# Kernel optimization log

Hardware: AMD Instinct MI355X
Metric: run time of the kernel (lower is better)

Reference implementation:

```python
import jax, jax.numpy as jnp
import numpy as np

N = 50000      # nodes
E = 1200000    # edges
G = 256        # graphs in batch
H = 64         # hidden_dim
F_IN = 5       # input_dim
L = 3          # num deep GCN layers
EPS_BN = 1e-5
EPS_MSG = 1e-7

def setup_inputs() -> dict:
    key = jax.random.key(0)
    ks = jax.random.split(key, 12)
    r = lambda i, shp, s=0.1: jax.random.normal(ks[i], shp, jnp.float32) * s
    return {
        "x": jax.random.normal(ks[0], (N, F_IN), jnp.float32),
        "edge_index": jax.random.randint(ks[1], (2, E), 0, N),
        "batch_idx": jnp.sort(jax.random.randint(ks[2], (N,), 0, G)),
        "conv1_W": r(3, (F_IN, H)), "conv1_b": jnp.zeros((H,), jnp.float32),
        "bn1_g": jnp.ones((H,), jnp.float32), "bn1_b": jnp.zeros((H,), jnp.float32),
        "ln_g": jnp.ones((L, H), jnp.float32), "ln_b": jnp.zeros((L, H), jnp.float32),
        "prelu_a": jnp.full((L, H), 0.25, jnp.float32),
        "gen_t": jnp.ones((L,), jnp.float32),
        "mlp_W1": r(4, (L, H, 2 * H)), "mlp_b1": jnp.zeros((L, 2 * H), jnp.float32),
        "mlp_bn_g": jnp.ones((L, 2 * H), jnp.float32), "mlp_bn_b": jnp.zeros((L, 2 * H), jnp.float32),
        "mlp_W2": r(5, (L, 2 * H, H)), "mlp_b2": jnp.zeros((L, H), jnp.float32),
        "lin1_W": r(6, ((L + 1) * H * 2, 2 * H)), "lin1_b": jnp.zeros((2 * H,), jnp.float32),
        "lin2_W": r(7, (2 * H, H)), "lin2_b": jnp.zeros((H,), jnp.float32),
        "out_W": r(8, (H, 1)), "out_b": jnp.zeros((1,), jnp.float32),
    }

def _layernorm(x, g, b):
    mu = jnp.mean(x, axis=-1, keepdims=True)
    var = jnp.mean(jnp.square(x - mu), axis=-1, keepdims=True)
    return (x - mu) * jax.lax.rsqrt(var + EPS_BN) * g + b

def _prelu(x, a):
    return jnp.where(x >= 0, x, a * x)

def _bn_eval(x, g, b):
    # eval-mode BatchNorm with running_mean=0, running_var=1
    return x * (g / jnp.sqrt(1.0 + EPS_BN)) + b

def reference(x, edge_index, batch_idx, conv1_W, conv1_b, bn1_g, bn1_b,
              ln_g, ln_b, prelu_a, gen_t, mlp_W1, mlp_b1, mlp_bn_g, mlp_bn_b,
              mlp_W2, mlp_b2, lin1_W, lin1_b, lin2_W, lin2_b, out_W, out_b):
    n = x.shape[0]
    src, dst = edge_index[0], edge_index[1]

    # ---- GCNConv (with self loops, symmetric normalization) ----
    loops = jnp.arange(n)
    row = jnp.concatenate([src, loops])  # [E+N]
    col = jnp.concatenate([dst, loops])
    h = x @ conv1_W
    deg = jax.ops.segment_sum(jnp.ones_like(col, jnp.float32), col, num_segments=n)
    dinv = jnp.where(deg > 0, deg ** -0.5, 0.0)
    norm = dinv[row] * dinv[col]
    h = jax.ops.segment_sum(h[row] * norm[:, None], col, num_segments=n) + conv1_b
    h = _bn_eval(h, bn1_g, bn1_b)
    h = jax.nn.relu(h)

    xs = [h]
    # ---- DeepGCNLayer (res+) x L, GENConv with softmax aggregation ----
    for i in range(ln_g.shape[0]):
        u = _layernorm(h, ln_g[i], ln_b[i])
        u = _prelu(u, prelu_a[i])
        msg = jax.nn.relu(u[src]) + EPS_MSG            # [E, H]
        sc = msg * gen_t[i]
        m = jax.ops.segment_max(sc, dst, num_segments=n)
        e = jnp.exp(sc - m[dst])
        s = jax.ops.segment_sum(e, dst, num_segments=n)
        alpha = e / s[dst]                             # segment-wise softmax per channel
        agg = jax.ops.segment_sum(msg * alpha, dst, num_segments=n) + u  # root add
        z = agg @ mlp_W1[i] + mlp_b1[i]
        z = _bn_eval(z, mlp_bn_g[i], mlp_bn_b[i])
        z = jax.nn.relu(z)
        z = z @ mlp_W2[i] + mlp_b2[i]
        h = h + z                                      # res+
        xs.append(h)

    # ---- JumpingKnowledge cat + global mean/max pool ----
    xc = jnp.concatenate(xs, axis=1)                   # [N, 4H]
    cnt = jax.ops.segment_sum(jnp.ones((n,), jnp.float32), batch_idx, num_segments=G)
    xmean = jax.ops.segment_sum(xc, batch_idx, num_segments=G) / jnp.maximum(cnt, 1.0)[:, None]
    xmax = jax.ops.segment_max(xc, batch_idx, num_segments=G)
    xmax = jnp.where(jnp.isfinite(xmax), xmax, 0.0)
    p = jnp.concatenate([xmean, xmax], axis=1)         # [G, 8H]

    # ---- readout MLP (dropout off in eval) ----
    p = jax.nn.relu(p @ lin1_W + lin1_b)
    p = jax.nn.relu(p @ lin2_W + lin2_b)
    return p @ out_W + out_b
```

## Files before the change

### kernel.cpp

```cpp
#include <hip/hip_runtime.h>
#include <math.h>

#define NND 50000
#define NE  1200000
#define NG  256
#define H   64
#define H2  128
#define H4  256
#define H8  512
#define FIN 5
#define EPS_BN 1e-5f
#define EPS_MSG 1e-7f
#define NB 196
#define TILES 196
#define TCAP 7168
#define EPB 4096
#define NB1 293
#define ELLC 72
#define PC 8
#define MT 64

typedef _Float16 half8 __attribute__((ext_vector_type(8)));
typedef _Float16 half4 __attribute__((ext_vector_type(4)));
typedef float floatx4 __attribute__((ext_vector_type(4)));


__global__ void k_setup(const int* __restrict__ batch, int* tilecur, int* __restrict__ gstart,
                        const float* __restrict__ x, float* __restrict__ xp,
                        const float* __restrict__ W1, const float* __restrict__ W2,
                        _Float16* __restrict__ w1f, _Float16* __restrict__ w2f) {
    int b = blockIdx.x, t = threadIdx.x;
    if (b < NB) {
        int n = b * 256 + t;
        if (n < NND) {
            float a0 = x[n * FIN + 0], a1 = x[n * FIN + 1], a2 = x[n * FIN + 2];
            float a3 = x[n * FIN + 3], a4 = x[n * FIN + 4];
            *(float4*)&xp[n * 8] = make_float4(a0, a1, a2, a3);
            *(float4*)&xp[n * 8 + 4] = make_float4(a4, 0.f, 0.f, 0.f);
        }
        return;
    }
    if (b == NB || b == NB + 1) {
        if (b == NB && t < TILES) tilecur[t] = 0;
        int g = (b - NB) * 256 + t;
        if (g > NG) return;
        int lo = 0, hi = NND;
        while (lo < hi) { int mid = (lo + hi) >> 1; if (batch[mid] < g) lo = mid + 1; else hi = mid; }
        gstart[g] = lo;
        return;
    }
    int tt = (b - NB - 2) * 256 + t;
    if (tt >= 3 * 16 * 64) return;
    int lane = tt & 63, fr = (tt >> 6) & 15, l = tt >> 10;
    {
        int jt = fr >> 1, kf = fr & 1;
        int j = jt * 16 + (lane & 15);
        int k0 = kf * 32 + (lane >> 4) * 8;
#pragma unroll
        for (int i = 0; i < 8; i++)
            w1f[(((size_t)l * 16 + jt * 2 + kf) * 64 + lane) * 8 + i] =
                (_Float16)W1[(size_t)l * H * H2 + (k0 + i) * H2 + j];
    }
    {
        int ct = fr >> 2, k2f = fr & 3;
        int c = ct * 16 + (lane & 15);
        int k0 = k2f * 32 + (lane >> 4) * 8;
#pragma unroll
        for (int i = 0; i < 8; i++)
            w2f[(((size_t)l * 16 + ct * 4 + k2f) * 64 + lane) * 8 + i] =
                (_Float16)W2[(size_t)l * H2 * H + (k0 + i) * H + c];
    }
}


__global__ void __launch_bounds__(256)
k_bin1(const int* __restrict__ ei, int* tilecur, unsigned* __restrict__ tilebuf) {
    __shared__ int cnt[TILES];
    __shared__ int base[TILES];
    int b = blockIdx.x, t = threadIdx.x;
    for (int i = t; i < TILES; i += 256) cnt[i] = 0;
    __syncthreads();
    int e0 = b * EPB;
#pragma unroll
    for (int r = 0; r < EPB / 256; r++) {
        int e = e0 + r * 256 + t;
        if (e < NE) atomicAdd(&cnt[ei[NE + e] >> 8], 1);
    }
    __syncthreads();
    for (int i = t; i < TILES; i += 256) {
        base[i] = atomicAdd(&tilecur[i], cnt[i]);
        cnt[i] = 0;
    }
    __syncthreads();
#pragma unroll
    for (int r = 0; r < EPB / 256; r++) {
        int e = e0 + r * 256 + t;
        if (e < NE) {
            int s = ei[e], d = ei[NE + e];
            int tile = d >> 8;
            int pos = base[tile] + atomicAdd(&cnt[tile], 1);
            if (pos < TCAP)
                tilebuf[(size_t)tile * TCAP + pos] = ((unsigned)s << 8) | (unsigned)(d & 255);
        }
    }
}

__global__ void __launch_bounds__(256)
k_bin2(const int* __restrict__ tilecur, const unsigned* __restrict__ tilebuf,
       unsigned short* __restrict__ ell, int* __restrict__ deg, float* __restrict__ dinv) {
    __shared__ unsigned short ell_l[256 * ELLC];
    __shared__ int cnt[256];
    int tile = blockIdx.x, t = threadIdx.x;
    cnt[t] = 0;
    __syncthreads();
    int n = min(tilecur[tile], TCAP);
    for (int i = t; i < n; i += 256) {
        unsigned v = tilebuf[(size_t)tile * TCAP + i];
        int dl = v & 255u;
        int slot = atomicAdd(&cnt[dl], 1);
        if (slot < ELLC) ell_l[dl * ELLC + slot] = (unsigned short)(v >> 8);
    }
    __syncthreads();
    const unsigned* s32 = (const unsigned*)ell_l;
    unsigned* d32 = (unsigned*)(ell + (size_t)tile * 256 * ELLC);
    for (int i = t; i < 256 * ELLC / 2; i += 256) d32[i] = s32[i];
    int d = tile * 256 + t;
    if (d < NND) {
        deg[d] = min(cnt[t], ELLC);
        dinv[d] = rsqrtf((float)cnt[t] + 1.0f);
    }
}


__global__ void k_gcn(const int* __restrict__ deg, const unsigned short* __restrict__ ell,
                      const float* __restrict__ xp, const float* __restrict__ dinv,
                      const float* __restrict__ W,
                      const float* __restrict__ cb, const float* __restrict__ bg,
                      const float* __restrict__ bb,
                      const float* __restrict__ lg, const float* __restrict__ lb,
                      const float* __restrict__ pa,
                      _Float16* __restrict__ xcH, _Float16* __restrict__ u_h) {
    int tid = blockIdx.x * blockDim.x + threadIdx.x;
    int d = tid >> 4;
    int r = threadIdx.x & 15;
    if (d >= NND) return;
    int dg = deg[d];
    size_t base = (size_t)d * ELLC;
    float xw0 = 0.f, xw1 = 0.f, xw2 = 0.f, xw3 = 0.f, xw4 = 0.f;
    for (int i = r; i < dg; i += 16) {
        int s = (int)ell[base + i];
        float dv = dinv[s];
        float4 a = *(const float4*)&xp[s * 8];
        float a4 = xp[s * 8 + 4];
        xw0 += a.x * dv; xw1 += a.y * dv; xw2 += a.z * dv;
        xw3 += a.w * dv; xw4 += a4 * dv;
    }
#pragma unroll
    for (int off = 1; off <= 8; off <<= 1) {
        xw0 += __shfl_xor(xw0, off, 64);
        xw1 += __shfl_xor(xw1, off, 64);
        xw2 += __shfl_xor(xw2, off, 64);
        xw3 += __shfl_xor(xw3, off, 64);
        xw4 += __shfl_xor(xw4, off, 64);
    }
    float dd = dinv[d];
    float4 xa = *(const float4*)&xp[d * 8];
    float xa4 = xp[d * 8 + 4];
    xw0 += dd * xa.x; xw1 += dd * xa.y; xw2 += dd * xa.z;
    xw3 += dd * xa.w; xw4 += dd * xa4;
    float bns = rsqrtf(1.f + EPS_BN);
    float x0[4];
    float sum = 0.f, sq = 0.f;
#pragma unroll
    for (int j = 0; j < 4; j++) {
        int c = 4 * r + j;
        float s_ = xw0 * W[c] + xw1 * W[H + c] + xw2 * W[2 * H + c]
                 + xw3 * W[3 * H + c] + xw4 * W[4 * H + c];
        float v = s_ * dd + cb[c];
        v = v * (bg[c] * bns) + bb[c];
        v = fmaxf(v, 0.f);
        x0[j] = v;
        sum += v; sq += v * v;
    }
    {
        half4 xh = {(_Float16)x0[0], (_Float16)x0[1], (_Float16)x0[2], (_Float16)x0[3]};
        *(half4*)&xcH[(size_t)d * H4 + 4 * r] = xh;
    }
#pragma unroll
    for (int off = 1; off <= 8; off <<= 1) {
        sum += __shfl_xor(sum, off, 64);
        sq  += __shfl_xor(sq,  off, 64);
    }
    float mu  = sum * (1.f / H);
    float var = sq * (1.f / H) - mu * mu;
    float rs = rsqrtf(var + EPS_BN);
    half4 yh;
#pragma unroll
    for (int j = 0; j < 4; j++) {
        int c = 4 * r + j;
        float y = (x0[j] - mu) * rs * lg[c] + lb[c];
        y = (y >= 0.f) ? y : pa[c] * y;
        yh[j] = (_Float16)y;
    }
    *(half4*)&u_h[(size_t)d * H + 4 * r] = yh;
}


__global__ void k_gen(const int* __restrict__ deg, const unsigned short* __restrict__ ell,
                      const _Float16* __restrict__ u_h,
                      const float* __restrict__ tptr, int li, _Float16* __restrict__ ua_h) {
    int d = (blockIdx.x * blockDim.x + threadIdx.x) >> 6;
    int lane = threadIdx.x & 63;
    if (d >= NND) return;
    int q = lane & 15, eg = lane >> 4;
    float t = tptr[li];
    int dg = deg[d];
    size_t base = (size_t)d * ELLC;
    half4 us = *(const half4*)&u_h[(size_t)d * H + 4 * q];
    float4 s4 = {0.f, 0.f, 0.f, 0.f}, n4 = {0.f, 0.f, 0.f, 0.f};
    for (int i0 = 0; i0 < dg; i0 += 64) {
        int idx = i0 + lane;
        int csrv = (idx < dg) ? (int)ell[base + idx] : 0;
        int chunk = min(64, dg - i0);
        for (int j = 0; j < chunk; j += 32) {
            half4 uv[8]; bool ok[8];
#pragma unroll
            for (int b2 = 0; b2 < 8; b2++) {
                int e_rel = j + 4 * b2 + eg;
                int s = __shfl(csrv, e_rel, 64);
                ok[b2] = (e_rel < chunk);
                uv[b2] = (half4){0, 0, 0, 0};
                if (ok[b2]) uv[b2] = *(const half4*)&u_h[(size_t)s * H + 4 * q];
            }
#pragma unroll
            for (int b2 = 0; b2 < 8; b2++) {
                if (ok[b2]) {
                    float m0 = fmaxf((float)uv[b2][0], 0.f) + EPS_MSG;
                    float m1 = fmaxf((float)uv[b2][1], 0.f) + EPS_MSG;
                    float m2 = fmaxf((float)uv[b2][2], 0.f) + EPS_MSG;
                    float m3 = fmaxf((float)uv[b2][3], 0.f) + EPS_MSG;
                    float e0 = __expf(m0 * t - 8.f);
                    float e1 = __expf(m1 * t - 8.f);
                    float e2 = __expf(m2 * t - 8.f);
                    float e3 = __expf(m3 * t - 8.f);
                    s4.x += e0; s4.y += e1; s4.z += e2; s4.w += e3;
                    n4.x += m0 * e0; n4.y += m1 * e1; n4.z += m2 * e2; n4.w += m3 * e3;
                }
            }
        }
    }
#pragma unroll
    for (int off = 16; off <= 32; off <<= 1) {
        s4.x += __shfl_xor(s4.x, off, 64); s4.y += __shfl_xor(s4.y, off, 64);
        s4.z += __shfl_xor(s4.z, off, 64); s4.w += __shfl_xor(s4.w, off, 64);
        n4.x += __shfl_xor(n4.x, off, 64); n4.y += __shfl_xor(n4.y, off, 64);
        n4.z += __shfl_xor(n4.z, off, 64); n4.w += __shfl_xor(n4.w, off, 64);
    }
    if (eg == 0) {
        float o0 = (float)us[0] + ((s4.x > 0.f) ? n4.x / s4.x : 0.f);
        float o1 = (float)us[1] + ((s4.y > 0.f) ? n4.y / s4.y : 0.f);
        float o2 = (float)us[2] + ((s4.z > 0.f) ? n4.z / s4.z : 0.f);
        float o3 = (float)us[3] + ((s4.w > 0.f) ? n4.w / s4.w : 0.f);
        half4 oh = {(_Float16)o0, (_Float16)o1, (_Float16)o2, (_Float16)o3};
        *(half4*)&ua_h[(size_t)d * H + 4 * q] = oh;
    }
}


__global__ void __launch_bounds__(256)
k_mlp(const _Float16* __restrict__ ua_h,
      const _Float16* __restrict__ w1f, const _Float16* __restrict__ w2f,
      const float* __restrict__ b1,
      const float* __restrict__ bng, const float* __restrict__ bnb,
      const float* __restrict__ b2,
      _Float16* __restrict__ xcH, int slice,
      const float* __restrict__ lg, const float* __restrict__ lb,
      const float* __restrict__ pa, _Float16* __restrict__ u_h, int do_ln) {
    __shared__ _Float16 a2[4][4][64][8];
    int t = threadIdx.x;
    int w = t >> 6, l = t & 63;
    int nb = blockIdx.x * MT;
    int c_in = l & 15, quad = l >> 4;
    bool wvalid = (nb + 16 * w) < NND;

    half8 af0 = {0,0,0,0,0,0,0,0}, af1 = af0;
    {
        int node = nb + 16 * w + c_in;
        if (node < NND) {
            af0 = *(const half8*)&u_h[0];
            af0 = *(const half8*)&ua_h[(size_t)node * H + quad * 8];
            af1 = *(const half8*)&ua_h[(size_t)node * H + 32 + quad * 8];
        }
    }

    floatx4 acc[8];
#pragma unroll
    for (int jt = 0; jt < 8; jt++) acc[jt] = (floatx4){0.f, 0.f, 0.f, 0.f};
#pragma unroll
    for (int jt = 0; jt < 8; jt++) {
        half8 bf0 = *(const half8*)&w1f[((size_t)(jt * 2 + 0) * 64 + l) * 8];
        half8 bf1 = *(const half8*)&w1f[((size_t)(jt * 2 + 1) * 64 + l) * 8];
        acc[jt] = __builtin_amdgcn_mfma_f32_16x16x32_f16(af0, bf0, acc[jt], 0, 0, 0);
        acc[jt] = __builtin_amdgcn_mfma_f32_16x16x32_f16(af1, bf1, acc[jt], 0, 0, 0);
    }

    {
        float bns = rsqrtf(1.f + EPS_BN);
#pragma unroll
        for (int jt = 0; jt < 8; jt++) {
            int j = jt * 16 + c_in;
            float b1v = b1[j], bsv = bng[j] * bns, bbv = bnb[j];
            int kf2 = jt >> 1;
            int lp = 16 * ((2 * jt + (c_in >> 3)) & 3);
            int ii = c_in & 7;
#pragma unroll
            for (int reg = 0; reg < 4; reg++) {
                float z = fmaxf((acc[jt][reg] + b1v) * bsv + bbv, 0.f);
                a2[w][kf2][quad * 4 + reg + lp][ii] = (_Float16)z;
            }
        }
    }

    floatx4 acc2[4];
#pragma unroll
    for (int ct = 0; ct < 4; ct++) acc2[ct] = (floatx4){0.f, 0.f, 0.f, 0.f};
    half8 a2f[4];
#pragma unroll
    for (int k2f = 0; k2f < 4; k2f++) a2f[k2f] = *(half8*)&a2[w][k2f][l][0];
#pragma unroll
    for (int ct = 0; ct < 4; ct++) {
#pragma unroll
        for (int k2f = 0; k2f < 4; k2f++) {
            half8 bfr = *(const half8*)&w2f[((size_t)(ct * 4 + k2f) * 64 + l) * 8];
            acc2[ct] = __builtin_amdgcn_mfma_f32_16x16x32_f16(a2f[k2f], bfr, acc2[ct], 0, 0, 0);
        }
    }

    float vv[4][4];
#pragma unroll
    for (int ct = 0; ct < 4; ct++) {
        int c = ct * 16 + c_in;
        float b2v = b2[c];
#pragma unroll
        for (int reg = 0; reg < 4; reg++) {
            int node = nb + 16 * w + quad * 4 + reg;
            float v = 0.f;
            if (wvalid) {
                v = (float)xcH[(size_t)node * H4 + slice * H + c] + acc2[ct][reg] + b2v;
                xcH[(size_t)node * H4 + (slice + 1) * H + c] = (_Float16)v;
            }
            vv[ct][reg] = v;
        }
    }
    if (do_ln) {
#pragma unroll
        for (int reg = 0; reg < 4; reg++) {
            float s = (vv[0][reg] + vv[1][reg]) + (vv[2][reg] + vv[3][reg]);
            float q = (vv[0][reg] * vv[0][reg] + vv[1][reg] * vv[1][reg]) +
                      (vv[2][reg] * vv[2][reg] + vv[3][reg] * vv[3][reg]);
#pragma unroll
            for (int off = 1; off <= 8; off <<= 1) {
                s += __shfl_xor(s, off, 64);
                q += __shfl_xor(q, off, 64);
            }
            float mu = s * (1.f / H);
            float var = q * (1.f / H) - mu * mu;
            float rs = rsqrtf(var + EPS_BN);
            int node = nb + 16 * w + quad * 4 + reg;
#pragma unroll
            for (int ct = 0; ct < 4; ct++) {
                int c = ct * 16 + c_in;
                float y = (vv[ct][reg] - mu) * rs * lg[c] + lb[c];
                y = (y >= 0.f) ? y : pa[c] * y;
                if (wvalid) u_h[(size_t)node * H + c] = (_Float16)y;
            }
        }
    }
}


__global__ void __launch_bounds__(256)
k_pool1(const _Float16* __restrict__ xcH, const int* __restrict__ gstart,
        float* __restrict__ psum_p, float* __restrict__ pmax_p) {
    __shared__ float4 ssum[256];
    __shared__ float4 smax[256];
    int b = blockIdx.x;
    int g = b >> 3, k = b & (PC - 1);
    int t = threadIdx.x;
    int start = gstart[g], end = gstart[g + 1];
    int len = end - start;
    int c0 = start + (len * k) / PC;
    int c1 = start + (len * (k + 1)) / PC;
    int q = t & 63, sub = t >> 6;
    float4 sum = {0.f, 0.f, 0.f, 0.f};
    float4 mx = {-INFINITY, -INFINITY, -INFINITY, -INFINITY};
    for (int n = c0 + sub; n < c1; n += 4) {
        half4 vh = *(const half4*)&xcH[(size_t)n * H4 + 4 * q];
        float v0 = (float)vh[0], v1 = (float)vh[1], v2 = (float)vh[2], v3 = (float)vh[3];
        sum.x += v0; sum.y += v1; sum.z += v2; sum.w += v3;
        mx.x = fmaxf(mx.x, v0); mx.y = fmaxf(mx.y, v1);
        mx.z = fmaxf(mx.z, v2); mx.w = fmaxf(mx.w, v3);
    }
    ssum[t] = sum; smax[t] = mx;
    __syncthreads();
    if (t < 64) {
        float4 s0 = ssum[t], s1 = ssum[t + 64], s2 = ssum[t + 128], s3 = ssum[t + 192];
        float4 m0 = smax[t], m1 = smax[t + 64], m2 = smax[t + 128], m3 = smax[t + 192];
        float4 S, M;
        S.x = (s0.x + s1.x) + (s2.x + s3.x);
        S.y = (s0.y + s1.y) + (s2.y + s3.y);
        S.z = (s0.z + s1.z) + (s2.z + s3.z);
        S.w = (s0.w + s1.w) + (s2.w + s3.w);
        M.x = fmaxf(fmaxf(m0.x, m1.x), fmaxf(m2.x, m3.x));
        M.y = fmaxf(fmaxf(m0.y, m1.y), fmaxf(m2.y, m3.y));
        M.z = fmaxf(fmaxf(m0.z, m1.z), fmaxf(m2.z, m3.z));
        M.w = fmaxf(fmaxf(m0.w, m1.w), fmaxf(m2.w, m3.w));
        *(float4*)&psum_p[(size_t)b * H4 + 4 * q] = S;
        *(float4*)&pmax_p[(size_t)b * H4 + 4 * q] = M;
    }
}

__global__ void __launch_bounds__(256)
k_readout(const float* __restrict__ psum_p, const float* __restrict__ pmax_p,
          const int* __restrict__ gstart,
          const float* __restrict__ W1, const float* __restrict__ b1,
          const float* __restrict__ W2, const float* __restrict__ b2,
          const float* __restrict__ Wo, const float* __restrict__ bo,
          float* __restrict__ out) {
    __shared__ float p0_l[H8];
    __shared__ float p1part[2][H2];
    __shared__ float p1_l[H2];
    __shared__ float p2part[4][H];
    __shared__ float p2_l[H];
    int g = blockIdx.x;
    int t = threadIdx.x;

    {
        float s = 0.f, m = -INFINITY;
#pragma unroll
        for (int k = 0; k < PC; k++) {
            s += psum_p[(size_t)(g * PC + k) * H4 + t];
            m = fmaxf(m, pmax_p[(size_t)(g * PC + k) * H4 + t]);
        }
        int cnt = gstart[g + 1] - gstart[g];
        p0_l[t] = s / fmaxf((float)cnt, 1.f);
        p0_l[H4 + t] = (cnt > 0) ? m : 0.f;
    }
    __syncthreads();

    {
        int j = t & 127, h = t >> 7;
        float acc = 0.f;
        int k0 = h * 256;
        for (int k = 0; k < 256; k++) acc += p0_l[k0 + k] * W1[(k0 + k) * H2 + j];
        p1part[h][j] = acc;
    }
    __syncthreads();
    if (t < H2) p1_l[t] = fmaxf(p1part[0][t] + p1part[1][t] + b1[t], 0.f);
    __syncthreads();

    {
        int c = t & 63, h = t >> 6;
        float acc = 0.f;
        int k0 = h * 32;
        for (int k = 0; k < 32; k++) acc += p1_l[k0 + k] * W2[(k0 + k) * H + c];
        p2part[h][c] = acc;
    }
    __syncthreads();
    if (t < H) p2_l[t] = fmaxf(((p2part[0][t] + p2part[1][t]) + (p2part[2][t] + p2part[3][t])) + b2[t], 0.f);
    __syncthreads();

    if (t < 64) {
        float v = p2_l[t] * Wo[t];
#pragma unroll
        for (int off = 32; off >= 1; off >>= 1) v += __shfl_xor(v, off, 64);
        if (t == 0) out[g] = v + bo[0];
    }
}

extern "C" void kernel_launch(void* const* d_in, const int* in_sizes, int n_in,
                              void* d_out, int out_size, void* d_ws, size_t ws_size,
                              hipStream_t stream) {
    const float* x       = (const float*)d_in[0];
    const int*   ei      = (const int*)d_in[1];
    const int*   batch   = (const int*)d_in[2];
    const float* conv1_W = (const float*)d_in[3];
    const float* conv1_b = (const float*)d_in[4];
    const float* bn1_g   = (const float*)d_in[5];
    const float* bn1_b   = (const float*)d_in[6];
    const float* ln_g    = (const float*)d_in[7];
    const float* ln_b    = (const float*)d_in[8];
    const float* prelu_a = (const float*)d_in[9];
    const float* gen_t   = (const float*)d_in[10];
    const float* mlp_W1  = (const float*)d_in[11];
    const float* mlp_b1  = (const float*)d_in[12];
    const float* mlp_bng = (const float*)d_in[13];
    const float* mlp_bnb = (const float*)d_in[14];
    const float* mlp_W2  = (const float*)d_in[15];
    const float* mlp_b2  = (const float*)d_in[16];
    const float* lin1_W  = (const float*)d_in[17];
    const float* lin1_b  = (const float*)d_in[18];
    const float* lin2_W  = (const float*)d_in[19];
    const float* lin2_b  = (const float*)d_in[20];
    const float* out_W   = (const float*)d_in[21];
    const float* out_b   = (const float*)d_in[22];
    float* out = (float*)d_out;

    float* ws   = (float*)d_ws;
    _Float16* xcH = (_Float16*)ws;
    float* xp   = (float*)(xcH + (size_t)NND * H4);
    float* dinv = xp + (size_t)NND * 8;
    int* deg    = (int*)(dinv + NND);
    int* gstart = deg + NND;
    int* tilecur = gstart + NG + 1;
    unsigned* tilebuf = (unsigned*)(tilecur + TILES);
    unsigned short* ell = (unsigned short*)(tilebuf + (size_t)TILES * TCAP);
    uintptr_t wb = (uintptr_t)(ell + (size_t)TILES * 256 * ELLC);
    wb = (wb + 15) & ~(uintptr_t)15;
    _Float16* w1f = (_Float16*)wb;
    _Float16* w2f = w1f + 3 * 8192;
    _Float16* u_h  = w2f + 3 * 8192;
    _Float16* ua_h = u_h + (size_t)NND * H;
    uintptr_t pb = (uintptr_t)(ua_h + (size_t)NND * H);
    pb = (pb + 15) & ~(uintptr_t)15;
    float* psum_p = (float*)pb;
    float* pmax_p = psum_p + (size_t)NG * PC * H4;

    const int B = 256;
    const int gGCN = (NND * 16 + B - 1) / B;
    const int gNH  = (NND * H) / B;
    const int gMLP = (NND + MT - 1) / MT;

    k_setup<<<NB + 2 + 12, B, 0, stream>>>(batch, tilecur, gstart, x, xp,
                                           mlp_W1, mlp_W2, w1f, w2f);
    k_bin1<<<NB1, B, 0, stream>>>(ei, tilecur, tilebuf);
    k_bin2<<<TILES, B, 0, stream>>>(tilecur, tilebuf, ell, deg, dinv);

    k_gcn<<<gGCN, B, 0, stream>>>(deg, ell, xp, dinv, conv1_W, conv1_b, bn1_g, bn1_b,
                                  ln_g, ln_b, prelu_a, xcH, u_h);

    for (int i = 0; i < 3; i++) {
        k_gen<<<gNH, B, 0, stream>>>(deg, ell, u_h, gen_t, i, ua_h);
        int do_ln = (i < 2) ? 1 : 0;
        k_mlp<<<gMLP, B, 0, stream>>>(ua_h,
                                      w1f + (size_t)i * 8192, w2f + (size_t)i * 8192,
                                      mlp_b1 + i * H2,
                                      mlp_bng + i * H2, mlp_bnb + i * H2,
                                      mlp_b2 + i * H,
                                      xcH, i,
                                      ln_g + (i + 1) * H, ln_b + (i + 1) * H,
                                      prelu_a + (i + 1) * H, u_h, do_ln);
    }

    k_pool1<<<NG * PC, B, 0, stream>>>(xcH, gstart, psum_p, pmax_p);
    k_readout<<<NG, B, 0, stream>>>(psum_p, pmax_p, gstart,
                                    lin1_W, lin1_b, lin2_W, lin2_b, out_W, out_b, out);
}
```

Measured before the change: 329.7 us.

## Build ELL adjacency directly with global atomics inside setup kernel

Replaces the two-pass tile binning (k_bin1/k_bin2 with an intermediate tile buffer and shared-memory ELL staging) with a direct scatter. Each edge atomically increments a per-node global counter and writes its source into the ELL slot, fused into k_setup after a memset. Degree and dinv arrays are dropped; consumers compute min(cnt, ELLC) and rsqrt(cnt+1) on the fly. This removes two kernel launches and the tilebuf round trip, at the cost of 1.2M contended global atomics and scattered 2-byte stores.

```diff
diff --git a/kernel.cpp b/kernel.cpp
--- a/kernel.cpp
+++ b/kernel.cpp
@@ -12,24 +12,35 @@
 #define EPS_BN 1e-5f
 #define EPS_MSG 1e-7f
 #define NB 196
-#define TILES 196
-#define TCAP 7168
-#define EPB 4096
-#define NB1 293
 #define ELLC 72
 #define PC 8
 #define MT 64
+#define EBLK 1172
 
 typedef _Float16 half8 __attribute__((ext_vector_type(8)));
 typedef _Float16 half4 __attribute__((ext_vector_type(4)));
 typedef float floatx4 __attribute__((ext_vector_type(4)));
 
 
-__global__ void k_setup(const int* __restrict__ batch, int* tilecur, int* __restrict__ gstart,
+__global__ void k_setup(const int* __restrict__ batch, int* __restrict__ cnt, int* __restrict__ gstart,
                         const float* __restrict__ x, float* __restrict__ xp,
                         const float* __restrict__ W1, const float* __restrict__ W2,
-                        _Float16* __restrict__ w1f, _Float16* __restrict__ w2f) {
+                        _Float16* __restrict__ w1f, _Float16* __restrict__ w2f,
+                        const int* __restrict__ ei, unsigned short* __restrict__ ell) {
     int b = blockIdx.x, t = threadIdx.x;
+    if (b >= NB + 14) {
+        int e0 = (b - NB - 14) * 1024 + t;
+#pragma unroll
+        for (int r = 0; r < 4; r++) {
+            int e = e0 + r * 256;
+            if (e < NE) {
+                int s = ei[e], d = ei[NE + e];
+                int slot = atomicAdd(&cnt[d], 1);
+                if (slot < ELLC) ell[(size_t)d * ELLC + slot] = (unsigned short)s;
+            }
+        }
+        return;
+    }
     if (b < NB) {
         int n = b * 256 + t;
         if (n < NND) {
@@ -41,7 +52,6 @@
         return;
     }
     if (b == NB || b == NB + 1) {
-        if (b == NB && t < TILES) tilecur[t] = 0;
         int g = (b - NB) * 256 + t;
         if (g > NG) return;
         int lo = 0, hi = NND;
@@ -73,67 +83,8 @@
 }
 
 
-__global__ void __launch_bounds__(256)
-k_bin1(const int* __restrict__ ei, int* tilecur, unsigned* __restrict__ tilebuf) {
-    __shared__ int cnt[TILES];
-    __shared__ int base[TILES];
-    int b = blockIdx.x, t = threadIdx.x;
-    for (int i = t; i < TILES; i += 256) cnt[i] = 0;
-    __syncthreads();
-    int e0 = b * EPB;
-#pragma unroll
-    for (int r = 0; r < EPB / 256; r++) {
-        int e = e0 + r * 256 + t;
-        if (e < NE) atomicAdd(&cnt[ei[NE + e] >> 8], 1);
-    }
-    __syncthreads();
-    for (int i = t; i < TILES; i += 256) {
-        base[i] = atomicAdd(&tilecur[i], cnt[i]);
-        cnt[i] = 0;
-    }
-    __syncthreads();
-#pragma unroll
-    for (int r = 0; r < EPB / 256; r++) {
-        int e = e0 + r * 256 + t;
-        if (e < NE) {
-            int s = ei[e], d = ei[NE + e];
-            int tile = d >> 8;
-            int pos = base[tile] + atomicAdd(&cnt[tile], 1);
-            if (pos < TCAP)
-                tilebuf[(size_t)tile * TCAP + pos] = ((unsigned)s << 8) | (unsigned)(d & 255);
-        }
-    }
-}
-
-__global__ void __launch_bounds__(256)
-k_bin2(const int* __restrict__ tilecur, const unsigned* __restrict__ tilebuf,
-       unsigned short* __restrict__ ell, int* __restrict__ deg, float* __restrict__ dinv) {
-    __shared__ unsigned short ell_l[256 * ELLC];
-    __shared__ int cnt[256];
-    int tile = blockIdx.x, t = threadIdx.x;
-    cnt[t] = 0;
-    __syncthreads();
-    int n = min(tilecur[tile], TCAP);
-    for (int i = t; i < n; i += 256) {
-        unsigned v = tilebuf[(size_t)tile * TCAP + i];
-        int dl = v & 255u;
-        int slot = atomicAdd(&cnt[dl], 1);
-        if (slot < ELLC) ell_l[dl * ELLC + slot] = (unsigned short)(v >> 8);
-    }
-    __syncthreads();
-    const unsigned* s32 = (const unsigned*)ell_l;
-    unsigned* d32 = (unsigned*)(ell + (size_t)tile * 256 * ELLC);
-    for (int i = t; i < 256 * ELLC / 2; i += 256) d32[i] = s32[i];
-    int d = tile * 256 + t;
-    if (d < NND) {
-        deg[d] = min(cnt[t], ELLC);
-        dinv[d] = rsqrtf((float)cnt[t] + 1.0f);
-    }
-}
-
-
-__global__ void k_gcn(const int* __restrict__ deg, const unsigned short* __restrict__ ell,
-                      const float* __restrict__ xp, const float* __restrict__ dinv,
+__global__ void k_gcn(const int* __restrict__ cnt, const unsigned short* __restrict__ ell,
+                      const float* __restrict__ xp,
                       const float* __restrict__ W,
                       const float* __restrict__ cb, const float* __restrict__ bg,
                       const float* __restrict__ bb,
@@ -144,12 +95,13 @@
     int d = tid >> 4;
     int r = threadIdx.x & 15;
     if (d >= NND) return;
-    int dg = deg[d];
+    int cr = cnt[d];
+    int dg = min(cr, ELLC);
     size_t base = (size_t)d * ELLC;
     float xw0 = 0.f, xw1 = 0.f, xw2 = 0.f, xw3 = 0.f, xw4 = 0.f;
     for (int i = r; i < dg; i += 16) {
         int s = (int)ell[base + i];
-        float dv = dinv[s];
+        float dv = rsqrtf((float)cnt[s] + 1.0f);
         float4 a = *(const float4*)&xp[s * 8];
         float a4 = xp[s * 8 + 4];
         xw0 += a.x * dv; xw1 += a.y * dv; xw2 += a.z * dv;
@@ -163,7 +115,7 @@
         xw3 += __shfl_xor(xw3, off, 64);
         xw4 += __shfl_xor(xw4, off, 64);
     }
-    float dd = dinv[d];
+    float dd = rsqrtf((float)cr + 1.0f);
     float4 xa = *(const float4*)&xp[d * 8];
     float xa4 = xp[d * 8 + 4];
     xw0 += dd * xa.x; xw1 += dd * xa.y; xw2 += dd * xa.z;
@@ -206,7 +158,7 @@
 }
 
 
-__global__ void k_gen(const int* __restrict__ deg, const unsigned short* __restrict__ ell,
+__global__ void k_gen(const int* __restrict__ cnt, const unsigned short* __restrict__ ell,
                       const _Float16* __restrict__ u_h,
                       const float* __restrict__ tptr, int li, _Float16* __restrict__ ua_h) {
     int d = (blockIdx.x * blockDim.x + threadIdx.x) >> 6;
@@ -214,7 +166,7 @@
     if (d >= NND) return;
     int q = lane & 15, eg = lane >> 4;
     float t = tptr[li];
-    int dg = deg[d];
+    int dg = min(cnt[d], ELLC);
     size_t base = (size_t)d * ELLC;
     half4 us = *(const half4*)&u_h[(size_t)d * H + 4 * q];
     float4 s4 = {0.f, 0.f, 0.f, 0.f}, n4 = {0.f, 0.f, 0.f, 0.f};
@@ -287,7 +239,6 @@
     {
         int node = nb + 16 * w + c_in;
         if (node < NND) {
-            af0 = *(const half8*)&u_h[0];
             af0 = *(const half8*)&ua_h[(size_t)node * H + quad * 8];
             af1 = *(const half8*)&ua_h[(size_t)node * H + 32 + quad * 8];
         }
@@ -509,13 +460,10 @@
     float* ws   = (float*)d_ws;
     _Float16* xcH = (_Float16*)ws;
     float* xp   = (float*)(xcH + (size_t)NND * H4);
-    float* dinv = xp + (size_t)NND * 8;
-    int* deg    = (int*)(dinv + NND);
-    int* gstart = deg + NND;
-    int* tilecur = gstart + NG + 1;
-    unsigned* tilebuf = (unsigned*)(tilecur + TILES);
-    unsigned short* ell = (unsigned short*)(tilebuf + (size_t)TILES * TCAP);
-    uintptr_t wb = (uintptr_t)(ell + (size_t)TILES * 256 * ELLC);
+    int* cnt    = (int*)(xp + (size_t)NND * 8);
+    int* gstart = cnt + NND;
+    unsigned short* ell = (unsigned short*)(gstart + NG + 1);
+    uintptr_t wb = (uintptr_t)(ell + (size_t)NND * ELLC);
     wb = (wb + 15) & ~(uintptr_t)15;
     _Float16* w1f = (_Float16*)wb;
     _Float16* w2f = w1f + 3 * 8192;
@@ -531,16 +479,15 @@
     const int gNH  = (NND * H) / B;
     const int gMLP = (NND + MT - 1) / MT;
 
-    k_setup<<<NB + 2 + 12, B, 0, stream>>>(batch, tilecur, gstart, x, xp,
-                                           mlp_W1, mlp_W2, w1f, w2f);
-    k_bin1<<<NB1, B, 0, stream>>>(ei, tilecur, tilebuf);
-    k_bin2<<<TILES, B, 0, stream>>>(tilecur, tilebuf, ell, deg, dinv);
-
-    k_gcn<<<gGCN, B, 0, stream>>>(deg, ell, xp, dinv, conv1_W, conv1_b, bn1_g, bn1_b,
+    hipMemsetAsync(cnt, 0, NND * sizeof(int), stream);
+    k_setup<<<NB + 14 + EBLK, B, 0, stream>>>(batch, cnt, gstart, x, xp,
+                                              mlp_W1, mlp_W2, w1f, w2f, ei, ell);
+
+    k_gcn<<<gGCN, B, 0, stream>>>(cnt, ell, xp, conv1_W, conv1_b, bn1_g, bn1_b,
                                   ln_g, ln_b, prelu_a, xcH, u_h);
 
     for (int i = 0; i < 3; i++) {
-        k_gen<<<gNH, B, 0, stream>>>(deg, ell, u_h, gen_t, i, ua_h);
+        k_gen<<<gNH, B, 0, stream>>>(cnt, ell, u_h, gen_t, i, ua_h);
         int do_ln = (i < 2) ? 1 : 0;
         k_mlp<<<gMLP, B, 0, stream>>>(ua_h,
                                       w1f + (size_t)i * 8192, w2f + (size_t)i * 8192,
```

Measured after the change: 390.5 us. 18.4% more time.

## Split node features into two 32-channel halves and run gather kernel per half

Applied to the files above, without the earlier changes.

The 64-channel fp16 node feature buffer is split into two separate 32-channel arrays, written by the GCN and MLP kernels. The softmax-aggregation gather kernel now runs twice per layer, once per half, with 8 edges handled in parallel per wave instead of 4. The gathered working set per pass is halved (3.2 MB per half), so it fits better in the on-chip caches during the random neighbour gather. The cost is double the kernel launches and twice the reads of the adjacency lists. A stray dummy load in the MLP kernel is also removed.

```diff
diff --git a/kernel.cpp b/kernel.cpp
--- a/kernel.cpp
+++ b/kernel.cpp
@@ -139,7 +139,8 @@
                       const float* __restrict__ bb,
                       const float* __restrict__ lg, const float* __restrict__ lb,
                       const float* __restrict__ pa,
-                      _Float16* __restrict__ xcH, _Float16* __restrict__ u_h) {
+                      _Float16* __restrict__ xcH,
+                      _Float16* __restrict__ u_hA, _Float16* __restrict__ u_hB) {
     int tid = blockIdx.x * blockDim.x + threadIdx.x;
     int d = tid >> 4;
     int r = threadIdx.x & 15;
@@ -202,55 +203,55 @@
         y = (y >= 0.f) ? y : pa[c] * y;
         yh[j] = (_Float16)y;
     }
-    *(half4*)&u_h[(size_t)d * H + 4 * r] = yh;
+    if (r < 8) *(half4*)&u_hA[(size_t)d * 32 + 4 * r] = yh;
+    else       *(half4*)&u_hB[(size_t)d * 32 + 4 * (r - 8)] = yh;
 }
 
 
 __global__ void k_gen(const int* __restrict__ deg, const unsigned short* __restrict__ ell,
-                      const _Float16* __restrict__ u_h,
-                      const float* __restrict__ tptr, int li, _Float16* __restrict__ ua_h) {
+                      const _Float16* __restrict__ u_src,
+                      const float* __restrict__ tptr, int li,
+                      _Float16* __restrict__ ua_h, int half_off) {
     int d = (blockIdx.x * blockDim.x + threadIdx.x) >> 6;
     int lane = threadIdx.x & 63;
     if (d >= NND) return;
-    int q = lane & 15, eg = lane >> 4;
+    int q = lane & 7, eg = lane >> 3;
     float t = tptr[li];
     int dg = deg[d];
     size_t base = (size_t)d * ELLC;
-    half4 us = *(const half4*)&u_h[(size_t)d * H + 4 * q];
+    half4 us = *(const half4*)&u_src[(size_t)d * 32 + 4 * q];
     float4 s4 = {0.f, 0.f, 0.f, 0.f}, n4 = {0.f, 0.f, 0.f, 0.f};
     for (int i0 = 0; i0 < dg; i0 += 64) {
         int idx = i0 + lane;
         int csrv = (idx < dg) ? (int)ell[base + idx] : 0;
         int chunk = min(64, dg - i0);
-        for (int j = 0; j < chunk; j += 32) {
-            half4 uv[8]; bool ok[8];
-#pragma unroll
-            for (int b2 = 0; b2 < 8; b2++) {
-                int e_rel = j + 4 * b2 + eg;
-                int s = __shfl(csrv, e_rel, 64);
-                ok[b2] = (e_rel < chunk);
-                uv[b2] = (half4){0, 0, 0, 0};
-                if (ok[b2]) uv[b2] = *(const half4*)&u_h[(size_t)s * H + 4 * q];
+        half4 uv[8]; bool ok[8];
+#pragma unroll
+        for (int b2 = 0; b2 < 8; b2++) {
+            int e_rel = 8 * b2 + eg;
+            int s = __shfl(csrv, e_rel, 64);
+            ok[b2] = (e_rel < chunk);
+            uv[b2] = (half4){0, 0, 0, 0};
+            if (ok[b2]) uv[b2] = *(const half4*)&u_src[(size_t)s * 32 + 4 * q];
+        }
+#pragma unroll
+        for (int b2 = 0; b2 < 8; b2++) {
+            if (ok[b2]) {
+                float m0 = fmaxf((float)uv[b2][0], 0.f) + EPS_MSG;
+                float m1 = fmaxf((float)uv[b2][1], 0.f) + EPS_MSG;
+                float m2 = fmaxf((float)uv[b2][2], 0.f) + EPS_MSG;
+                float m3 = fmaxf((float)uv[b2][3], 0.f) + EPS_MSG;
+                float e0 = __expf(m0 * t - 8.f);
+                float e1 = __expf(m1 * t - 8.f);
+                float e2 = __expf(m2 * t - 8.f);
+                float e3 = __expf(m3 * t - 8.f);
+                s4.x += e0; s4.y += e1; s4.z += e2; s4.w += e3;
+                n4.x += m0 * e0; n4.y += m1 * e1; n4.z += m2 * e2; n4.w += m3 * e3;
             }
-#pragma unroll
-            for (int b2 = 0; b2 < 8; b2++) {
-                if (ok[b2]) {
-                    float m0 = fmaxf((float)uv[b2][0], 0.f) + EPS_MSG;
-                    float m1 = fmaxf((float)uv[b2][1], 0.f) + EPS_MSG;
-                    float m2 = fmaxf((float)uv[b2][2], 0.f) + EPS_MSG;
-                    float m3 = fmaxf((float)uv[b2][3], 0.f) + EPS_MSG;
-                    float e0 = __expf(m0 * t - 8.f);
-                    float e1 = __expf(m1 * t - 8.f);
-                    float e2 = __expf(m2 * t - 8.f);
-                    float e3 = __expf(m3 * t - 8.f);
-                    s4.x += e0; s4.y += e1; s4.z += e2; s4.w += e3;
-                    n4.x += m0 * e0; n4.y += m1 * e1; n4.z += m2 * e2; n4.w += m3 * e3;
-                }
-            }
-        }
-    }
-#pragma unroll
-    for (int off = 16; off <= 32; off <<= 1) {
+        }
+    }
+#pragma unroll
+    for (int off = 8; off <= 32; off <<= 1) {
         s4.x += __shfl_xor(s4.x, off, 64); s4.y += __shfl_xor(s4.y, off, 64);
         s4.z += __shfl_xor(s4.z, off, 64); s4.w += __shfl_xor(s4.w, off, 64);
         n4.x += __shfl_xor(n4.x, off, 64); n4.y += __shfl_xor(n4.y, off, 64);
@@ -262,7 +263,7 @@
         float o2 = (float)us[2] + ((s4.z > 0.f) ? n4.z / s4.z : 0.f);
         float o3 = (float)us[3] + ((s4.w > 0.f) ? n4.w / s4.w : 0.f);
         half4 oh = {(_Float16)o0, (_Float16)o1, (_Float16)o2, (_Float16)o3};
-        *(half4*)&ua_h[(size_t)d * H + 4 * q] = oh;
+        *(half4*)&ua_h[(size_t)d * H + half_off + 4 * q] = oh;
     }
 }
 
@@ -275,7 +276,8 @@
       const float* __restrict__ b2,
       _Float16* __restrict__ xcH, int slice,
       const float* __restrict__ lg, const float* __restrict__ lb,
-      const float* __restrict__ pa, _Float16* __restrict__ u_h, int do_ln) {
+      const float* __restrict__ pa,
+      _Float16* __restrict__ u_hA, _Float16* __restrict__ u_hB, int do_ln) {
     __shared__ _Float16 a2[4][4][64][8];
     int t = threadIdx.x;
     int w = t >> 6, l = t & 63;
@@ -287,7 +289,6 @@
     {
         int node = nb + 16 * w + c_in;
         if (node < NND) {
-            af0 = *(const half8*)&u_h[0];
             af0 = *(const half8*)&ua_h[(size_t)node * H + quad * 8];
             af1 = *(const half8*)&ua_h[(size_t)node * H + 32 + quad * 8];
         }
@@ -372,7 +373,10 @@
                 int c = ct * 16 + c_in;
                 float y = (vv[ct][reg] - mu) * rs * lg[c] + lb[c];
                 y = (y >= 0.f) ? y : pa[c] * y;
-                if (wvalid) u_h[(size_t)node * H + c] = (_Float16)y;
+                if (wvalid) {
+                    if (ct < 2) u_hA[(size_t)node * 32 + ct * 16 + c_in] = (_Float16)y;
+                    else        u_hB[(size_t)node * 32 + (ct - 2) * 16 + c_in] = (_Float16)y;
+                }
             }
         }
     }
@@ -519,8 +523,9 @@
     wb = (wb + 15) & ~(uintptr_t)15;
     _Float16* w1f = (_Float16*)wb;
     _Float16* w2f = w1f + 3 * 8192;
-    _Float16* u_h  = w2f + 3 * 8192;
-    _Float16* ua_h = u_h + (size_t)NND * H;
+    _Float16* u_hA = w2f + 3 * 8192;
+    _Float16* u_hB = u_hA + (size_t)NND * 32;
+    _Float16* ua_h = u_hB + (size_t)NND * 32;
     uintptr_t pb = (uintptr_t)(ua_h + (size_t)NND * H);
     pb = (pb + 15) & ~(uintptr_t)15;
     float* psum_p = (float*)pb;
@@ -537,10 +542,11 @@
     k_bin2<<<TILES, B, 0, stream>>>(tilecur, tilebuf, ell, deg, dinv);
 
     k_gcn<<<gGCN, B, 0, stream>>>(deg, ell, xp, dinv, conv1_W, conv1_b, bn1_g, bn1_b,
-                                  ln_g, ln_b, prelu_a, xcH, u_h);
+                                  ln_g, ln_b, prelu_a, xcH, u_hA, u_hB);
 
     for (int i = 0; i < 3; i++) {
-        k_gen<<<gNH, B, 0, stream>>>(deg, ell, u_h, gen_t, i, ua_h);
+        k_gen<<<gNH, B, 0, stream>>>(deg, ell, u_hA, gen_t, i, ua_h, 0);
+        k_gen<<<gNH, B, 0, stream>>>(deg, ell, u_hB, gen_t, i, ua_h, 32);
         int do_ln = (i < 2) ? 1 : 0;
         k_mlp<<<gMLP, B, 0, stream>>>(ua_h,
                                       w1f + (size_t)i * 8192, w2f + (size_t)i * 8192,
@@ -549,7 +555,7 @@
                                       mlp_b2 + i * H,
                                       xcH, i,
                                       ln_g + (i + 1) * H, ln_b + (i + 1) * H,
-                                      prelu_a + (i + 1) * H, u_h, do_ln);
+                                      prelu_a + (i + 1) * H, u_hA, u_hB, do_ln);
     }
 
     k_pool1<<<NG * PC, B, 0, stream>>>(xcH, gstart, psum_p, pmax_p);
```

After: 376.3 us. 1.14x slower.
